# Kernel optimization log

Measured on AMD Instinct MI355X. Metric: run time of the kernel, lower is better.

The kernel has to match this reference:

```python
import jax, jax.numpy as jnp
import numpy as np

N_EMBED = 256
N_HEADS = 4
HEAD_SIZE = N_EMBED // N_HEADS  # 64
BLOCK_SIZE = 768
LN_EPS = 1e-5


def layer_norm(x, g, b):
    mu = jnp.mean(x, axis=-1, keepdims=True)
    var = jnp.var(x, axis=-1, keepdims=True)
    return (x - mu) * jax.lax.rsqrt(var + LN_EPS) * g + b


def setup_inputs() -> dict:
    key = jax.random.key(0)
    ks = jax.random.split(key, 12)
    B, T, C, H, hs = 32, BLOCK_SIZE, N_EMBED, N_HEADS, HEAD_SIZE
    s_in = 1.0 / np.sqrt(C)
    s_ff = 1.0 / np.sqrt(4 * C)
    return {
        "x": jax.random.normal(ks[0], (B, T, C), jnp.float32),
        # per-head projections, stacked: [H, C, hs]
        "Wq": jax.random.normal(ks[1], (H, C, hs), jnp.float32) * s_in,
        "Wk": jax.random.normal(ks[2], (H, C, hs), jnp.float32) * s_in,
        "Wv": jax.random.normal(ks[3], (H, C, hs), jnp.float32) * s_in,
        "Wo": jax.random.normal(ks[4], (C, C), jnp.float32) * s_in,
        "bo": jnp.zeros((C,), jnp.float32),
        "W1": jax.random.normal(ks[5], (C, 4 * C), jnp.float32) * s_in,
        "b1": jnp.zeros((4 * C,), jnp.float32),
        "W2": jax.random.normal(ks[6], (4 * C, C), jnp.float32) * s_ff,
        "b2": jnp.zeros((C,), jnp.float32),
        "g1": jnp.ones((C,), jnp.float32),
        "be1": jnp.zeros((C,), jnp.float32),
        "g2": jnp.ones((C,), jnp.float32),
        "be2": jnp.zeros((C,), jnp.float32),
    }


def reference(x, Wq, Wk, Wv, Wo, bo, W1, b1, W2, b2, g1, be1, g2, be2):
    B, T, C = x.shape
    # --- multi-head causal self-attention (pre-LN) ---
    h = layer_norm(x, g1, be1)
    q = jnp.einsum("btc,hcd->bhtd", h, Wq)
    k = jnp.einsum("btc,hcd->bhtd", h, Wk)
    v = jnp.einsum("btc,hcd->bhtd", h, Wv)
    scores = jnp.einsum("bhtd,bhsd->bhts", q, k) * (HEAD_SIZE ** -0.5)
    causal = jnp.tril(jnp.ones((T, T), bool))
    scores = jnp.where(causal, scores, -jnp.inf)
    attn = jax.nn.softmax(scores, axis=-1)  # dropout = identity (eval)
    o = jnp.einsum("bhts,bhsd->bhtd", attn, v)
    o = o.transpose(0, 2, 1, 3).reshape(B, T, C)  # concat heads
    x = x + o @ Wo + bo
    # --- feed-forward (pre-LN) ---
    h2 = layer_norm(x, g2, be2)
    x = x + jax.nn.relu(h2 @ W1 + b1) @ W2 + b2
    return x
```

## Files before the change

kernel.cpp:

```cpp
#include <hip/hip_runtime.h>
#include <stdint.h>

using short8   = __attribute__((ext_vector_type(8))) short;
using f32x4    = __attribute__((ext_vector_type(4))) float;
using ushort4v = __attribute__((ext_vector_type(4))) unsigned short;
using uint2v   = __attribute__((ext_vector_type(2))) unsigned int;

#define CSC  0.1803368801111f
#define FIXC 20.0f

__device__ __forceinline__ unsigned short f2bf(float f) {
    unsigned int u = __builtin_bit_cast(unsigned int, f);
    u += 0x7FFFu + ((u >> 16) & 1u);
    return (unsigned short)(u >> 16);
}
__device__ __forceinline__ float bf2f(unsigned short s) {
    unsigned int u = ((unsigned int)s) << 16;
    return __builtin_bit_cast(float, u);
}
__device__ __forceinline__ unsigned pk2bf(float a, float b) {
    unsigned r;
    asm("v_cvt_pk_bf16_f32 %0, %1, %2" : "=v"(r) : "v"(a), "v"(b));
    return r;
}

__device__ __forceinline__ void gload16(const void* g, void* l) {
    __builtin_amdgcn_global_load_lds(
        (const __attribute__((address_space(1))) void*)(uintptr_t)g,
        (__attribute__((address_space(3))) void*)(unsigned)(uintptr_t)l,
        16, 0, 0);
}

__device__ __forceinline__ uint2v ln_row_pk(f32x4 v, f32x4 gv, f32x4 bvv) {
    float s  = v[0] + v[1] + v[2] + v[3];
    float s2 = v[0]*v[0] + v[1]*v[1] + v[2]*v[2] + v[3]*v[3];
    for (int m = 1; m < 64; m <<= 1) {
        s  += __shfl_xor(s,  m, 64);
        s2 += __shfl_xor(s2, m, 64);
    }
    float mu  = s * (1.0f / 256.0f);
    float var = s2 * (1.0f / 256.0f) - mu * mu;
    float rs  = rsqrtf(var + 1e-5f);
    float r0 = (v[0] - mu) * rs * gv[0] + bvv[0];
    float r1 = (v[1] - mu) * rs * gv[1] + bvv[1];
    float r2 = (v[2] - mu) * rs * gv[2] + bvv[2];
    float r3 = (v[3] - mu) * rs * gv[3] + bvv[3];
    uint2v u; u[0] = pk2bf(r0, r1); u[1] = pk2bf(r2, r3);
    return u;
}

__global__ __launch_bounds__(256) void prep_k(const float* __restrict__ x, const float* __restrict__ g1,
                                              const float* __restrict__ be1, unsigned short* __restrict__ h,
                                              const float* __restrict__ Wq, const float* __restrict__ Wk,
                                              const float* __restrict__ Wv, const float* __restrict__ Wo,
                                              const float* __restrict__ W1, const float* __restrict__ W2,
                                              unsigned short* __restrict__ wpackT, unsigned short* __restrict__ woT,
                                              unsigned short* __restrict__ w1T, unsigned short* __restrict__ w2T) {
    __shared__ float t[64][65];
    if (blockIdx.x >= 192) {
        int row  = (blockIdx.x - 192) * 4 + (threadIdx.x >> 6);
        int lane = threadIdx.x & 63;
        f32x4 v = *(const f32x4*)(x + (size_t)row * 256 + lane * 4);
        f32x4 gv = *(const f32x4*)(g1 + lane * 4);
        f32x4 bv = *(const f32x4*)(be1 + lane * 4);
        uint2v u = ln_row_pk(v, gv, bv);
        *(uint2v*)(h + (size_t)row * 256 + lane * 4) = u;
        return;
    }
    const int bid = blockIdx.x;
    const float* in; unsigned short* out;
    int R, C, r0, c0;
    if (bid < 48) {
        int z = bid >> 2, cx = bid & 3;
        int qkv = z >> 2, hh = z & 3;
        in = ((qkv == 0) ? Wq : (qkv == 1) ? Wk : Wv) + (size_t)hh * 256 * 64;
        out = wpackT + (size_t)(qkv * 256 + hh * 64) * 256;
        R = 256; C = 64; r0 = cx * 64; c0 = 0;
    } else if (bid < 64) {
        int tt = bid - 48;
        in = Wo; out = woT; R = 256; C = 256; r0 = (tt >> 2) * 64; c0 = (tt & 3) * 64;
    } else if (bid < 128) {
        int tt = bid - 64;
        in = W1; out = w1T; R = 256; C = 1024; r0 = (tt & 3) * 64; c0 = (tt >> 2) * 64;
    } else {
        int tt = bid - 128;
        in = W2; out = w2T; R = 1024; C = 256; r0 = (tt & 15) * 64; c0 = (tt >> 4) * 64;
    }
    const int tx = threadIdx.x & 63, ty = threadIdx.x >> 6;
    #pragma unroll
    for (int i = 0; i < 64; i += 4)
        t[i + ty][tx] = in[(size_t)(r0 + i + ty) * C + c0 + tx];
    __syncthreads();
    #pragma unroll
    for (int i = 0; i < 64; i += 4)
        out[(size_t)(c0 + i + ty) * R + r0 + tx] = f2bf(t[tx][i + ty]);
}

__global__ __launch_bounds__(256) void qkv_k(const unsigned short* __restrict__ h,
                                             const unsigned short* __restrict__ wpackT,
                                             unsigned short* __restrict__ qk,
                                             unsigned short* __restrict__ vT) {
    __shared__ unsigned short As[128 * 64];
    __shared__ unsigned short Bs[128 * 64];
    const int tid  = threadIdx.x;
    const int lane = tid & 63;
    const int w    = tid >> 6;
    const int wm   = w >> 1, wn = w & 1;
    const int l15  = lane & 15, l4 = lane >> 4;
    const int bid  = blockIdx.x;

    const unsigned short *A, *BT;
    unsigned short* outp;
    int bm, bn, N;
    float qsc = 1.0f;
    if (bid < 768) {
        const int xcd = bid & 7, i = bid >> 3;
        bm = xcd * 24 + (i >> 2);
        bn = i & 3;
        A = h; BT = wpackT; outp = qk; N = 512;
        if (bn < 2) qsc = CSC;
    } else {
        const int t = bid - 768;
        const int xcd = t & 7, j = t >> 3;
        bn = xcd * 24 + (j >> 1);
        bm = j & 1;
        A = wpackT + 512 * 256; BT = h; outp = vT; N = 24576;
    }
    const int K = 256;

    f32x4 acc[4][4] = {};

    const size_t K2 = (size_t)K * 2;
    const int i0   = w * 4096 + lane * 16;
    const int row0 = i0 >> 7;
    const int cb0  = (i0 & 127) ^ ((row0 & 7) << 4);
    const char* aSrc = (const char*)A  + ((size_t)(bm * 128 + row0)) * K2 + cb0;
    const char* bSrc = (const char*)BT + ((size_t)(bn * 128 + row0)) * K2 + cb0;

    for (int t = 0; t < 4; ++t) {
        {
            const char* aS = aSrc + (size_t)t * 128;
            const char* bS = bSrc + (size_t)t * 128;
            char* aD = (char*)&As[0] + w * 4096;
            char* bD = (char*)&Bs[0] + w * 4096;
            #pragma unroll
            for (int c = 0; c < 4; ++c) {
                gload16(aS + (size_t)c * 8 * K2, aD + c * 1024);
                gload16(bS + (size_t)c * 8 * K2, bD + c * 1024);
            }
        }
        __syncthreads();
        #pragma unroll
        for (int kf = 0; kf < 2; ++kf) {
            int kb = kf * 64 + l4 * 16;
            short8 af[4], bfr[4];
            #pragma unroll
            for (int mf = 0; mf < 4; ++mf) {
                int row = wm * 64 + mf * 16 + l15;
                af[mf] = *(const short8*)((const char*)&As[0] + ((row * 128 + kb) ^ ((row & 7) << 4)));
            }
            #pragma unroll
            for (int nf = 0; nf < 4; ++nf) {
                int row = wn * 64 + nf * 16 + l15;
                bfr[nf] = *(const short8*)((const char*)&Bs[0] + ((row * 128 + kb) ^ ((row & 7) << 4)));
            }
            #pragma unroll
            for (int mf = 0; mf < 4; ++mf)
                #pragma unroll
                for (int nf = 0; nf < 4; ++nf)
                    acc[mf][nf] = __builtin_amdgcn_mfma_f32_16x16x32_bf16(af[mf], bfr[nf], acc[mf][nf], 0, 0, 0);
        }
        __syncthreads();
    }

    #pragma unroll
    for (int nf = 0; nf < 4; ++nf) {
        int col = bn * 128 + wn * 64 + nf * 16 + l15;
        #pragma unroll
        for (int mf = 0; mf < 4; ++mf) {
            int row0o = bm * 128 + wm * 64 + mf * 16 + l4 * 4;
            size_t off = (size_t)row0o * N + col;
            unsigned p01 = pk2bf(acc[mf][nf][0] * qsc, acc[mf][nf][1] * qsc);
            unsigned p23 = pk2bf(acc[mf][nf][2] * qsc, acc[mf][nf][3] * qsc);
            outp[off]                 = (unsigned short)p01;
            outp[off + (size_t)N]     = (unsigned short)(p01 >> 16);
            outp[off + (size_t)N * 2] = (unsigned short)p23;
            outp[off + (size_t)N * 3] = (unsigned short)(p23 >> 16);
        }
    }
}

template <int EPI, bool DB>
__global__ __launch_bounds__(256) void gemm_bt(const unsigned short* __restrict__ A,
                                               const unsigned short* __restrict__ BT,
                                               void* __restrict__ outp,
                                               const float* __restrict__ bias,
                                               const void* __restrict__ resid,
                                               int K, int N) {
    __shared__ unsigned short As[DB ? 2 : 1][128 * 64];
    __shared__ unsigned short Bs[DB ? 2 : 1][128 * 64];
    const int tid  = threadIdx.x;
    const int lane = tid & 63;
    const int w    = tid >> 6;
    const int wm   = w >> 1, wn = w & 1;
    const int bm   = blockIdx.y, bn = blockIdx.x;
    const int l15  = lane & 15, l4 = lane >> 4;

    f32x4 acc[4][4] = {};

    const size_t K2 = (size_t)K * 2;
    const int i0   = w * 4096 + lane * 16;
    const int row0 = i0 >> 7;
    const int cb0  = (i0 & 127) ^ ((row0 & 7) << 4);
    const char* aSrc = (const char*)A  + ((size_t)(bm * 128 + row0)) * K2 + cb0;
    const char* bSrc = (const char*)BT + ((size_t)(bn * 128 + row0)) * K2 + cb0;
    const int nt = K >> 6;

    auto stage = [&](int t, int buf) {
        const char* aS = aSrc + (size_t)t * 128;
        const char* bS = bSrc + (size_t)t * 128;
        char* aD = (char*)&As[buf][0] + w * 4096;
        char* bD = (char*)&Bs[buf][0] + w * 4096;
        #pragma unroll
        for (int c = 0; c < 4; ++c) {
            gload16(aS + (size_t)c * 8 * K2, aD + c * 1024);
            gload16(bS + (size_t)c * 8 * K2, bD + c * 1024);
        }
    };
    auto compute = [&](int buf) {
        const char* AsB = (const char*)&As[buf][0];
        const char* BsB = (const char*)&Bs[buf][0];
        #pragma unroll
        for (int kf = 0; kf < 2; ++kf) {
            int kb = kf * 64 + l4 * 16;
            short8 af[4], bfr[4];
            #pragma unroll
            for (int mf = 0; mf < 4; ++mf) {
                int row = wm * 64 + mf * 16 + l15;
                af[mf] = *(const short8*)(AsB + ((row * 128 + kb) ^ ((row & 7) << 4)));
            }
            #pragma unroll
            for (int nf = 0; nf < 4; ++nf) {
                int row = wn * 64 + nf * 16 + l15;
                bfr[nf] = *(const short8*)(BsB + ((row * 128 + kb) ^ ((row & 7) << 4)));
            }
            #pragma unroll
            for (int mf = 0; mf < 4; ++mf)
                #pragma unroll
                for (int nf = 0; nf < 4; ++nf)
                    acc[mf][nf] = __builtin_amdgcn_mfma_f32_16x16x32_bf16(af[mf], bfr[nf], acc[mf][nf], 0, 0, 0);
        }
    };

    if (DB) {
        stage(0, 0);
        for (int t = 0; t < nt; ++t) {
            const int cur = t & 1;
            __syncthreads();
            if (t + 1 < nt) stage(t + 1, cur ^ 1);
            compute(cur);
        }
    } else {
        for (int t = 0; t < nt; ++t) {
            stage(t, 0);
            __syncthreads();
            compute(0);
            __syncthreads();
        }
    }

    #pragma unroll
    for (int nf = 0; nf < 4; ++nf) {
        int col = bn * 128 + wn * 64 + nf * 16 + l15;
        float bv = bias[col];
        #pragma unroll
        for (int mf = 0; mf < 4; ++mf) {
            int row0o = bm * 128 + wm * 64 + mf * 16 + l4 * 4;
            size_t off = (size_t)row0o * N + col;
            float v[4];
            #pragma unroll
            for (int r = 0; r < 4; ++r)
                v[r] = acc[mf][nf][r] + bv + ((const float*)resid)[off + (size_t)r * N];
            unsigned short* O = (unsigned short*)outp;
            unsigned p01 = pk2bf(v[0], v[1]), p23 = pk2bf(v[2], v[3]);
            O[off]                 = (unsigned short)p01;
            O[off + (size_t)N]     = (unsigned short)(p01 >> 16);
            O[off + (size_t)N * 2] = (unsigned short)p23;
            O[off + (size_t)N * 3] = (unsigned short)(p23 >> 16);
        }
    }
}

__global__ __launch_bounds__(256) void ff_fused(const unsigned short* __restrict__ x1b,
                                                const float* __restrict__ g2,
                                                const float* __restrict__ be2,
                                                const unsigned short* __restrict__ w1T,
                                                const unsigned short* __restrict__ w2T,
                                                const float* __restrict__ b1,
                                                const float* __restrict__ b2,
                                                float* __restrict__ out) {
    __shared__ unsigned short sA[4][96 * 64];
    __shared__ unsigned short sW1[16384];
    __shared__ unsigned short sW2[16384];
    __shared__ unsigned short sAct[96 * 64];
    const int tid = threadIdx.x, lane = tid & 63, w = tid >> 6;
    const int l15 = lane & 15, l4 = lane >> 4;
    const int wm = w >> 1, wn = w & 1;
    const int r0 = blockIdx.x * 96;

    {
        f32x4 gv = *(const f32x4*)(g2 + lane * 4);
        f32x4 bv = *(const f32x4*)(be2 + lane * 4);
        const int ks = lane >> 4, colb = (lane & 15) * 8;
        #pragma unroll
        for (int it = 0; it < 24; ++it) {
            int row = it * 4 + w;
            ushort4v u4 = *(const ushort4v*)(x1b + (size_t)(r0 + row) * 256 + lane * 4);
            f32x4 v;
            #pragma unroll
            for (int q = 0; q < 4; ++q) v[q] = bf2f(u4[q]);
            uint2v u = ln_row_pk(v, gv, bv);
            *(uint2v*)((char*)&sA[0][0] + ks * 12288 + row * 128 + (colb ^ ((row & 7) << 4))) = u;
        }
    }

    auto stage_w1 = [&](int c) {
        const char* wb = (const char*)w1T + (size_t)(c * 64) * 512;
        #pragma unroll
        for (int g = 0; g < 8; ++g) {
            int j = g * 4096 + tid * 16;
            int ks = j >> 13, row = (j >> 7) & 63, cb = j & 127;
            gload16(wb + (size_t)row * 512 + ks * 128 + (cb ^ ((row & 7) << 4)),
                    (char*)&sW1[0] + j);
        }
    };
    auto stage_w2 = [&](int c) {
        const char* wb = (const char*)w2T + (size_t)c * 128;
        #pragma unroll
        for (int g = 0; g < 8; ++g) {
            int j = g * 4096 + tid * 16;
            int row = j >> 7, cb = j & 127;
            gload16(wb + (size_t)row * 2048 + (cb ^ ((row & 7) << 4)),
                    (char*)&sW2[0] + j);
        }
    };

    stage_w1(0);
    __syncthreads();

    short8 hfr[3][4][2];
    #pragma unroll
    for (int mf = 0; mf < 3; ++mf) {
        const int row = wm * 48 + mf * 16 + l15;
        #pragma unroll
        for (int ks = 0; ks < 4; ++ks)
            #pragma unroll
            for (int kf = 0; kf < 2; ++kf) {
                const int kb = kf * 64 + l4 * 16;
                hfr[mf][ks][kf] = *(const short8*)((const char*)&sA[0][0] + ks * 12288
                                    + ((row * 128 + kb) ^ ((row & 7) << 4)));
            }
    }

    f32x4 oacc[3][8] = {};

    for (int c = 0; c < 16; ++c) {
        stage_w2(c);

        f32x4 aacc[3][2] = {};
        __builtin_amdgcn_s_setprio(1);
        #pragma unroll
        for (int ks = 0; ks < 4; ++ks) {
            #pragma unroll
            for (int kf = 0; kf < 2; ++kf) {
                const int kb = kf * 64 + l4 * 16;
                short8 wf[2];
                #pragma unroll
                for (int nf = 0; nf < 2; ++nf) {
                    int row = wn * 32 + nf * 16 + l15;
                    wf[nf] = *(const short8*)((const char*)&sW1[0] + ks * 8192
                               + ((row * 128 + kb) ^ ((row & 7) << 4)));
                }
                #pragma unroll
                for (int mf = 0; mf < 3; ++mf)
                    #pragma unroll
                    for (int nf = 0; nf < 2; ++nf)
                        aacc[mf][nf] = __builtin_amdgcn_mfma_f32_16x16x32_bf16(wf[nf], hfr[mf][ks][kf], aacc[mf][nf], 0, 0, 0);
            }
        }
        __builtin_amdgcn_s_setprio(0);
        #pragma unroll
        for (int mf = 0; mf < 3; ++mf)
            #pragma unroll
            for (int nf = 0; nf < 2; ++nf) {
                int nl = wn * 32 + nf * 16 + l4 * 4;
                f32x4 bv = *(const f32x4*)(b1 + c * 64 + nl);
                float v0 = aacc[mf][nf][0] + bv[0]; v0 = v0 > 0.0f ? v0 : 0.0f;
                float v1 = aacc[mf][nf][1] + bv[1]; v1 = v1 > 0.0f ? v1 : 0.0f;
                float v2 = aacc[mf][nf][2] + bv[2]; v2 = v2 > 0.0f ? v2 : 0.0f;
                float v3 = aacc[mf][nf][3] + bv[3]; v3 = v3 > 0.0f ? v3 : 0.0f;
                uint2v u; u[0] = pk2bf(v0, v1); u[1] = pk2bf(v2, v3);
                int m = wm * 48 + mf * 16 + l15;
                *(uint2v*)((char*)&sAct[0] + ((m * 128 + nl * 2) ^ ((m & 7) << 4))) = u;
            }

        __syncthreads();

        if (c + 1 < 16) stage_w1(c + 1);

        __builtin_amdgcn_s_setprio(1);
        #pragma unroll
        for (int kf = 0; kf < 2; ++kf) {
            const int kb = kf * 64 + l4 * 16;
            short8 af[3], wf[8];
            #pragma unroll
            for (int mf = 0; mf < 3; ++mf) {
                int m = wm * 48 + mf * 16 + l15;
                af[mf] = *(const short8*)((const char*)&sAct[0] + ((m * 128 + kb) ^ ((m & 7) << 4)));
            }
            #pragma unroll
            for (int nf = 0; nf < 8; ++nf) {
                int n2 = wn * 128 + nf * 16 + l15;
                wf[nf] = *(const short8*)((const char*)&sW2[0] + ((n2 * 128 + kb) ^ ((n2 & 7) << 4)));
            }
            #pragma unroll
            for (int mf = 0; mf < 3; ++mf)
                #pragma unroll
                for (int nf = 0; nf < 8; ++nf)
                    oacc[mf][nf] = __builtin_amdgcn_mfma_f32_16x16x32_bf16(af[mf], wf[nf], oacc[mf][nf], 0, 0, 0);
        }
        __builtin_amdgcn_s_setprio(0);

        __syncthreads();
    }

    #pragma unroll
    for (int nf = 0; nf < 8; ++nf) {
        const int col = wn * 128 + nf * 16 + l15;
        const float bv = b2[col];
        #pragma unroll
        for (int mf = 0; mf < 3; ++mf) {
            const int row = r0 + wm * 48 + mf * 16 + l4 * 4;
            const size_t off = (size_t)row * 256 + col;
            #pragma unroll
            for (int r = 0; r < 4; ++r)
                out[off + (size_t)r * 256] = oacc[mf][nf][r] + bv + bf2f(x1b[off + (size_t)r * 256]);
        }
    }
}

__global__ __launch_bounds__(256) void attn_k(const unsigned short* __restrict__ qk,
                                              const unsigned short* __restrict__ vT,
                                              unsigned short* __restrict__ o) {
    __shared__ unsigned short Ks[2][64 * 64];
    __shared__ unsigned short Vt[2][64 * 64];
    __shared__ unsigned short Pl[4][16 * 64];
    const int tid = threadIdx.x, lane = tid & 63, w = tid >> 6;
    const int l15 = lane & 15, l4 = lane >> 4;
    const int gid = blockIdx.x;
    const int xcd = gid & 7, slot = gid >> 3;
    const int sl6 = slot / 6;
    const int bh  = xcd * 16 + sl6;
    const int x   = slot - sl6 * 6;
    const int qb1 = x, qb2 = 11 - x;
    const int b = bh >> 2, h = bh & 3;
    const unsigned short* Qb = qk + (size_t)b * 768 * 512 + h * 64;
    const char* Kg = (const char*)(Qb + 256);
    const char* Vg = (const char*)(vT + (size_t)(h * 64) * 24576 + (size_t)b * 768);
    const int t01 = qb1 * 64, t02 = qb2 * 64;
    const int tq1 = t01 + w * 16 + l15;
    const int tq2 = t02 + w * 16 + l15;

    short8 q1f0 = *(const short8*)(Qb + (size_t)tq1 * 512 + l4 * 8);
    short8 q1f1 = *(const short8*)(Qb + (size_t)tq1 * 512 + 32 + l4 * 8);
    short8 q2f0 = *(const short8*)(Qb + (size_t)tq2 * 512 + l4 * 8);
    short8 q2f1 = *(const short8*)(Qb + (size_t)tq2 * 512 + 32 + l4 * 8);

    const int srow = w * 16 + (lane >> 3);
    const int scb  = ((lane & 7) * 16) ^ ((srow & 7) << 4);
    const char* kSrc = Kg + (size_t)srow * 1024 + scb;
    const char* vSrc = Vg + (size_t)srow * 49152 + scb;
    char* kDst0 = (char*)&Ks[0][0] + w * 2048;
    char* vDst0 = (char*)&Vt[0][0] + w * 2048;

    f32x4 oA[4] = {}, oB[4] = {};
    float lsA = 0.0f, lsB = 0.0f;
    unsigned short* Pw = &Pl[w][0];
    const char* KsB;
    const char* VtB;
    int sb = 0;

    auto do_tile = [&](short8 qf0, short8 qf1, f32x4 (&oacc)[4], float& lsum, bool diag, int tq) {
        f32x4 sacc[4] = {};
        __builtin_amdgcn_s_setprio(1);
        #pragma unroll
        for (int kf = 0; kf < 2; ++kf) {
            const int kb = kf * 64 + l4 * 16;
            short8 qf = kf ? qf1 : qf0;
            #pragma unroll
            for (int nf = 0; nf < 4; ++nf) {
                int sr = nf * 16 + l15;
                short8 kfr = *(const short8*)(KsB + ((sr * 128 + kb) ^ ((sr & 7) << 4)));
                sacc[nf] = __builtin_amdgcn_mfma_f32_16x16x32_bf16(kfr, qf, sacc[nf], 0, 0, 0);
            }
        }
        __builtin_amdgcn_s_setprio(0);

        if (diag) {
            #pragma unroll
            for (int nf = 0; nf < 4; ++nf)
                #pragma unroll
                for (int r = 0; r < 4; ++r) {
                    int s = sb * 64 + nf * 16 + l4 * 4 + r;
                    if (s > tq) sacc[nf][r] = -1e30f;
                }
        }
        float psum = 0.0f;
        #pragma unroll
        for (int nf = 0; nf < 4; ++nf) {
            float p0 = __builtin_amdgcn_exp2f(sacc[nf][0] - FIXC);
            float p1 = __builtin_amdgcn_exp2f(sacc[nf][1] - FIXC);
            float p2 = __builtin_amdgcn_exp2f(sacc[nf][2] - FIXC);
            float p3 = __builtin_amdgcn_exp2f(sacc[nf][3] - FIXC);
            psum += (p0 + p1) + (p2 + p3);
            uint2v u; u[0] = pk2bf(p0, p1); u[1] = pk2bf(p2, p3);
            *(uint2v*)((char*)Pw + ((l15 * 128 + nf * 32 + l4 * 8) ^ ((l15 & 7) << 4))) = u;
        }
        psum += __shfl_xor(psum, 16, 64);
        psum += __shfl_xor(psum, 32, 64);
        lsum += psum;

        __builtin_amdgcn_s_setprio(1);
        #pragma unroll
        for (int kf = 0; kf < 2; ++kf) {
            const int kb = kf * 64 + l4 * 16;
            short8 pa = *(const short8*)((const char*)Pw + ((l15 * 128 + kb) ^ ((l15 & 7) << 4)));
            #pragma unroll
            for (int nf = 0; nf < 4; ++nf) {
                int dr = nf * 16 + l15;
                short8 vfr = *(const short8*)(VtB + ((dr * 128 + kb) ^ ((dr & 7) << 4)));
                oacc[nf] = __builtin_amdgcn_mfma_f32_16x16x32_bf16(pa, vfr, oacc[nf], 0, 0, 0);
            }
        }
        __builtin_amdgcn_s_setprio(0);
    };

    gload16(kSrc, kDst0);                 gload16(kSrc + 8 * 1024, kDst0 + 1024);
    gload16(vSrc, vDst0);                 gload16(vSrc + 8 * 49152, vDst0 + 1024);

    for (sb = 0; sb <= qb2; ++sb) {
        const int pb = sb & 1;
        __syncthreads();
        if (sb < qb2) {
            const char* ks = kSrc + (size_t)(sb + 1) * 65536;
            const char* vs = vSrc + (size_t)(sb + 1) * 128;
            char* kd = kDst0 + (pb ^ 1) * 8192;
            char* vd = vDst0 + (pb ^ 1) * 8192;
            gload16(ks, kd);              gload16(ks + 8 * 1024, kd + 1024);
            gload16(vs, vd);              gload16(vs + 8 * 49152, vd + 1024);
        }
        KsB = (const char*)&Ks[0][0] + pb * 8192;
        VtB = (const char*)&Vt[0][0] + pb * 8192;

        do_tile(q2f0, q2f1, oB, lsB, sb == qb2, tq2);
        if (sb <= qb1) do_tile(q1f0, q1f1, oA, lsA, sb == qb1, tq1);
    }

    float liA = 1.0f / lsA, liB = 1.0f / lsB;
    float lrA[4], lrB[4];
    #pragma unroll
    for (int r = 0; r < 4; ++r) {
        lrA[r] = __shfl(liA, l4 * 4 + r, 64);
        lrB[r] = __shfl(liB, l4 * 4 + r, 64);
    }
    const int tA = t01 + w * 16 + l4 * 4;
    const int tB = t02 + w * 16 + l4 * 4;
    unsigned short* oa = o + ((size_t)(b * 768 + tA)) * 256 + h * 64;
    unsigned short* ob = o + ((size_t)(b * 768 + tB)) * 256 + h * 64;
    #pragma unroll
    for (int nf = 0; nf < 4; ++nf) {
        unsigned a01 = pk2bf(oA[nf][0] * lrA[0], oA[nf][1] * lrA[1]);
        unsigned a23 = pk2bf(oA[nf][2] * lrA[2], oA[nf][3] * lrA[3]);
        unsigned b01 = pk2bf(oB[nf][0] * lrB[0], oB[nf][1] * lrB[1]);
        unsigned b23 = pk2bf(oB[nf][2] * lrB[2], oB[nf][3] * lrB[3]);
        oa[nf * 16 + l15]       = (unsigned short)a01;
        oa[256 + nf * 16 + l15] = (unsigned short)(a01 >> 16);
        oa[512 + nf * 16 + l15] = (unsigned short)a23;
        oa[768 + nf * 16 + l15] = (unsigned short)(a23 >> 16);
        ob[nf * 16 + l15]       = (unsigned short)b01;
        ob[256 + nf * 16 + l15] = (unsigned short)(b01 >> 16);
        ob[512 + nf * 16 + l15] = (unsigned short)b23;
        ob[768 + nf * 16 + l15] = (unsigned short)(b23 >> 16);
    }
}

extern "C" void kernel_launch(void* const* d_in, const int* in_sizes, int n_in,
                              void* d_out, int out_size, void* d_ws, size_t ws_size,
                              hipStream_t stream) {
    const float* x   = (const float*)d_in[0];
    const float* Wq  = (const float*)d_in[1];
    const float* Wk  = (const float*)d_in[2];
    const float* Wv  = (const float*)d_in[3];
    const float* Wo  = (const float*)d_in[4];
    const float* bo  = (const float*)d_in[5];
    const float* W1  = (const float*)d_in[6];
    const float* b1  = (const float*)d_in[7];
    const float* W2  = (const float*)d_in[8];
    const float* b2  = (const float*)d_in[9];
    const float* g1  = (const float*)d_in[10];
    const float* be1 = (const float*)d_in[11];
    const float* g2  = (const float*)d_in[12];
    const float* be2 = (const float*)d_in[13];

    char* ws = (char*)d_ws;
    unsigned short* qk_ws  = (unsigned short*)(ws + 0);
    unsigned short* vT_ws  = (unsigned short*)(ws + 25165824);
    unsigned short* o_ws   = (unsigned short*)(ws + 37748736);
    unsigned short* h_ws   = (unsigned short*)(ws + 50331648);
    unsigned short* x1b_ws = (unsigned short*)(ws + 62914560);
    unsigned short* wpackT = (unsigned short*)(ws + 88080384);
    unsigned short* woT    = (unsigned short*)(ws + 88473600);
    unsigned short* w1T    = (unsigned short*)(ws + 88604672);
    unsigned short* w2T    = (unsigned short*)(ws + 89128960);

    prep_k<<<6336, 256, 0, stream>>>(x, g1, be1, h_ws, Wq, Wk, Wv, Wo, W1, W2, wpackT, woT, w1T, w2T);
    qkv_k<<<1152, 256, 0, stream>>>(h_ws, wpackT, qk_ws, vT_ws);
    attn_k<<<768, 256, 0, stream>>>(qk_ws, vT_ws, o_ws);
    gemm_bt<2, true><<<dim3(2, 192), 256, 0, stream>>>(o_ws, woT, x1b_ws, bo, x, 256, 256);
    ff_fused<<<256, 256, 0, stream>>>(x1b_ws, g2, be2, w1T, w2T, b1, b2, (float*)d_out);
}
```

Measured before the change: 112.0 us.

## Double-buffer W1/W2 chunk staging in fused FF kernel with vmcnt-based waits

Replaces the single-buffered W1/W2 LDS staging in the fused feed-forward kernel with double buffers in one shared LDS arena. W1 is prefetched two chunks ahead and W2 one chunk ahead, and the full __syncthreads is replaced by explicit lgkmcnt/vmcnt waits plus a raw barrier, so global loads overlap the MFMA work. The b1 bias is also staged into LDS once. LDS use grows to 144 KB, which limits occupancy to one block per CU, and the hand-counted vmcnt values must match the number of in-flight loads exactly.

```diff
diff --git a/kernel.cpp b/kernel.cpp
--- a/kernel.cpp
+++ b/kernel.cpp
@@ -8,6 +8,10 @@
 
 #define CSC  0.1803368801111f
 #define FIXC 20.0f
+
+#define WAITLG()   asm volatile("s_waitcnt lgkmcnt(0)" ::: "memory")
+#define WAITVM(n)  asm volatile("s_waitcnt vmcnt(" #n ")" ::: "memory")
+#define BAR()      __builtin_amdgcn_s_barrier()
 
 __device__ __forceinline__ unsigned short f2bf(float f) {
     unsigned int u = __builtin_bit_cast(unsigned int, f);
@@ -299,10 +303,7 @@
                                                 const float* __restrict__ b1,
                                                 const float* __restrict__ b2,
                                                 float* __restrict__ out) {
-    __shared__ unsigned short sA[4][96 * 64];
-    __shared__ unsigned short sW1[16384];
-    __shared__ unsigned short sW2[16384];
-    __shared__ unsigned short sAct[96 * 64];
+    __shared__ __align__(16) char smem[147456];
     const int tid = threadIdx.x, lane = tid & 63, w = tid >> 6;
     const int l15 = lane & 15, l4 = lane >> 4;
     const int wm = w >> 1, wn = w & 1;
@@ -320,53 +321,62 @@
             #pragma unroll
             for (int q = 0; q < 4; ++q) v[q] = bf2f(u4[q]);
             uint2v u = ln_row_pk(v, gv, bv);
-            *(uint2v*)((char*)&sA[0][0] + ks * 12288 + row * 128 + (colb ^ ((row & 7) << 4))) = u;
-        }
-    }
-
-    auto stage_w1 = [&](int c) {
+            *(uint2v*)(smem + ks * 12288 + row * 128 + (colb ^ ((row & 7) << 4))) = u;
+        }
+    }
+    WAITLG(); BAR();
+
+    short8 hfr[3][4][2];
+    #pragma unroll
+    for (int mf = 0; mf < 3; ++mf) {
+        const int row = wm * 48 + mf * 16 + l15;
+        #pragma unroll
+        for (int ks = 0; ks < 4; ++ks)
+            #pragma unroll
+            for (int kf = 0; kf < 2; ++kf) {
+                const int kb = kf * 64 + l4 * 16;
+                hfr[mf][ks][kf] = *(const short8*)(smem + ks * 12288
+                                    + ((row * 128 + kb) ^ ((row & 7) << 4)));
+            }
+    }
+    WAITLG(); BAR();
+
+    auto stage_w1 = [&](int c, int buf) {
         const char* wb = (const char*)w1T + (size_t)(c * 64) * 512;
         #pragma unroll
         for (int g = 0; g < 8; ++g) {
             int j = g * 4096 + tid * 16;
             int ks = j >> 13, row = (j >> 7) & 63, cb = j & 127;
             gload16(wb + (size_t)row * 512 + ks * 128 + (cb ^ ((row & 7) << 4)),
-                    (char*)&sW1[0] + j);
+                    smem + buf * 32768 + j);
         }
     };
-    auto stage_w2 = [&](int c) {
+    auto stage_w2 = [&](int c, int buf) {
         const char* wb = (const char*)w2T + (size_t)c * 128;
         #pragma unroll
         for (int g = 0; g < 8; ++g) {
             int j = g * 4096 + tid * 16;
             int row = j >> 7, cb = j & 127;
             gload16(wb + (size_t)row * 2048 + (cb ^ ((row & 7) << 4)),
-                    (char*)&sW2[0] + j);
+                    smem + 65536 + buf * 32768 + j);
         }
     };
 
-    stage_w1(0);
-    __syncthreads();
-
-    short8 hfr[3][4][2];
-    #pragma unroll
-    for (int mf = 0; mf < 3; ++mf) {
-        const int row = wm * 48 + mf * 16 + l15;
-        #pragma unroll
-        for (int ks = 0; ks < 4; ++ks)
-            #pragma unroll
-            for (int kf = 0; kf < 2; ++kf) {
-                const int kb = kf * 64 + l4 * 16;
-                hfr[mf][ks][kf] = *(const short8*)((const char*)&sA[0][0] + ks * 12288
-                                    + ((row * 128 + kb) ^ ((row & 7) << 4)));
-            }
-    }
-
+    gload16((const char*)b1 + tid * 16, smem + 143360 + tid * 16);
+    stage_w1(0, 0);
+    stage_w2(0, 0);
+    stage_w1(1, 1);
+
+    const float* sB1f = (const float*)(smem + 143360);
     f32x4 oacc[3][8] = {};
 
     for (int c = 0; c < 16; ++c) {
-        stage_w2(c);
-
+        WAITLG();
+        if (c < 15) { WAITVM(16); } else { WAITVM(8); }
+        BAR();
+        if (c + 1 < 16) stage_w2(c + 1, (c + 1) & 1);
+
+        const char* W1B = smem + (c & 1) * 32768;
         f32x4 aacc[3][2] = {};
         __builtin_amdgcn_s_setprio(1);
         #pragma unroll
@@ -378,7 +388,7 @@
                 #pragma unroll
                 for (int nf = 0; nf < 2; ++nf) {
                     int row = wn * 32 + nf * 16 + l15;
-                    wf[nf] = *(const short8*)((const char*)&sW1[0] + ks * 8192
+                    wf[nf] = *(const short8*)(W1B + ks * 8192
                                + ((row * 128 + kb) ^ ((row & 7) << 4)));
                 }
                 #pragma unroll
@@ -394,20 +404,22 @@
             #pragma unroll
             for (int nf = 0; nf < 2; ++nf) {
                 int nl = wn * 32 + nf * 16 + l4 * 4;
-                f32x4 bv = *(const f32x4*)(b1 + c * 64 + nl);
+                f32x4 bv = *(const f32x4*)(sB1f + c * 64 + nl);
                 float v0 = aacc[mf][nf][0] + bv[0]; v0 = v0 > 0.0f ? v0 : 0.0f;
                 float v1 = aacc[mf][nf][1] + bv[1]; v1 = v1 > 0.0f ? v1 : 0.0f;
                 float v2 = aacc[mf][nf][2] + bv[2]; v2 = v2 > 0.0f ? v2 : 0.0f;
                 float v3 = aacc[mf][nf][3] + bv[3]; v3 = v3 > 0.0f ? v3 : 0.0f;
                 uint2v u; u[0] = pk2bf(v0, v1); u[1] = pk2bf(v2, v3);
                 int m = wm * 48 + mf * 16 + l15;
-                *(uint2v*)((char*)&sAct[0] + ((m * 128 + nl * 2) ^ ((m & 7) << 4))) = u;
-            }
-
-        __syncthreads();
-
-        if (c + 1 < 16) stage_w1(c + 1);
-
+                *(uint2v*)(smem + 131072 + ((m * 128 + nl * 2) ^ ((m & 7) << 4))) = u;
+            }
+
+        WAITLG();
+        if (c < 15) { WAITVM(16); } else { WAITVM(0); }
+        BAR();
+        if (c + 2 < 16) stage_w1(c + 2, c & 1);
+
+        const char* W2B = smem + 65536 + (c & 1) * 32768;
         __builtin_amdgcn_s_setprio(1);
         #pragma unroll
         for (int kf = 0; kf < 2; ++kf) {
@@ -416,12 +428,12 @@
             #pragma unroll
             for (int mf = 0; mf < 3; ++mf) {
                 int m = wm * 48 + mf * 16 + l15;
-                af[mf] = *(const short8*)((const char*)&sAct[0] + ((m * 128 + kb) ^ ((m & 7) << 4)));
+                af[mf] = *(const short8*)(smem + 131072 + ((m * 128 + kb) ^ ((m & 7) << 4)));
             }
             #pragma unroll
             for (int nf = 0; nf < 8; ++nf) {
                 int n2 = wn * 128 + nf * 16 + l15;
-                wf[nf] = *(const short8*)((const char*)&sW2[0] + ((n2 * 128 + kb) ^ ((n2 & 7) << 4)));
+                wf[nf] = *(const short8*)(W2B + ((n2 * 128 + kb) ^ ((n2 & 7) << 4)));
             }
             #pragma unroll
             for (int mf = 0; mf < 3; ++mf)
@@ -430,8 +442,6 @@
                     oacc[mf][nf] = __builtin_amdgcn_mfma_f32_16x16x32_bf16(af[mf], wf[nf], oacc[mf][nf], 0, 0, 0);
         }
         __builtin_amdgcn_s_setprio(0);
-
-        __syncthreads();
     }
 
     #pragma unroll
```

After: 110.0 us. Within noise of the previous version (-1.8%).
